# Performance work log

Hardware: AMD Instinct MI355X
Metric: run time of the kernel (lower is better)

## Reference

```python
import jax, jax.numpy as jnp
import numpy as np

TEMPERATURE = 0.1
NUM_CLASSES = 100


def setup_inputs() -> dict:
    key = jax.random.key(0)
    k1, k2 = jax.random.split(key)
    embeddings = jax.random.normal(k1, (8192, 128), dtype=jnp.float32)
    labels = jax.random.randint(k2, (8192,), 0, NUM_CLASSES, dtype=jnp.int64)
    return {"embeddings": embeddings, "labels": labels}


def reference(embeddings, labels):
    # L2-normalize rows (eps matches torch.nn.functional.normalize clamp)
    norm = jnp.maximum(jnp.linalg.norm(embeddings, axis=1, keepdims=True), 1e-12)
    e = embeddings / norm
    sim = jnp.matmul(e, e.T) / TEMPERATURE  # [N, N]
    n = sim.shape[0]
    eye = jnp.eye(n, dtype=bool)
    # positives: same label, excluding self
    pos = (labels[None, :] == labels[:, None]) & ~eye
    # The per-row torch loop computes soft-target cross-entropy over all
    # non-diagonal entries: row_loss_i = -sum_{j in pos(i)} log_softmax(sim[i, j!=i])_j.
    # log_softmax is permutation-invariant, so concatenation order is irrelevant.
    neg_inf = jnp.finfo(sim.dtype).min
    masked = jnp.where(eye, neg_inf, sim)
    logz = jax.nn.logsumexp(masked, axis=1, keepdims=True)  # [N, 1]
    logp = sim - logz  # [N, N]
    row_loss = -jnp.sum(jnp.where(pos, logp, 0.0), axis=1)  # rows with no positives contribute 0
    return jnp.sum(row_loss) / n
```

## Files before the change

### kernel.cpp

```cpp
#include <hip/hip_runtime.h>


#define N 8192
#define D 128
#define NCLS 100
#define JSPLIT 32
#define IBLK 256
#define NJT ((N / JSPLIT) / 16)
#define NPART 8
#define K2E 14.4269504088896340736f
#define LN2 0.69314718055994530942f

typedef __bf16 bf16x8 __attribute__((ext_vector_type(8)));
typedef float f32x4 __attribute__((ext_vector_type(4)));

#define EBF_OFF 0u
#define INV_OFF 0x200000u
#define CNT_OFF 0x208000u
#define Z_OFF   0x208200u
#define SP_OFF  0x210200u
#define ZERO_SZ (512u + 32768u + (NPART * NCLS * D * 4u))

__device__ __forceinline__ unsigned short f32_to_bf16_rne(float f) {
    unsigned int u = __float_as_uint(f);
    u += 0x7fffu + ((u >> 16) & 1u);
    return (unsigned short)(u >> 16);
}


__global__ __launch_bounds__(256) void prep_kernel(
        const float* __restrict__ emb, const int* __restrict__ labels,
        unsigned char* __restrict__ ebf, int* __restrict__ cnt,
        float* __restrict__ spart) {
    const int wave = threadIdx.x >> 6;
    const int lane = threadIdx.x & 63;
    const int row  = blockIdx.x * 4 + wave;

    const float2 v = *(const float2*)(emb + (size_t)row * D + lane * 2);
    float ss = v.x * v.x + v.y * v.y;
    #pragma unroll
    for (int off = 32; off; off >>= 1) ss += __shfl_xor(ss, off);
    const float inv = 1.0f / fmaxf(sqrtf(ss), 1e-12f);
    const float ex = v.x * inv, ey = v.y * inv;

    const int grp = row >> 4, col = row & 15;
    const int c = lane >> 4, q = (lane >> 2) & 3, j2 = lane & 3;
    unsigned int packed = (unsigned int)f32_to_bf16_rne(ex) |
                          ((unsigned int)f32_to_bf16_rne(ey) << 16);
    *(unsigned int*)(ebf + grp * 4096 + c * 1024 + q * 256 + col * 16 + j2 * 4) = packed;

    const int lab = labels[row];
    float* sp = spart + (size_t)(row & (NPART - 1)) * (NCLS * D)
                      + (size_t)lab * D + lane * 2;
    atomicAdd(sp, ex);
    atomicAdd(sp + 1, ey);

    if (lane == 0) atomicAdd(&cnt[lab], 1);
}

__global__ __launch_bounds__(256) void zsum_kernel(
        const unsigned char* __restrict__ ebf, float* __restrict__ z) {
    const int t    = threadIdx.x;
    const int w    = t >> 6;
    const int lane = t & 63;
    const int q    = lane >> 4;
    const int col  = lane & 15;
    const int iw   = blockIdx.x * IBLK + w * 64;
    const int jb   = blockIdx.y * (N / JSPLIT);

    bf16x8 a[4][4];
    #pragma unroll
    for (int g = 0; g < 4; ++g) {
        const unsigned char* ag = ebf + (size_t)(iw / 16 + g) * 4096 + lane * 16;
        #pragma unroll
        for (int c = 0; c < 4; ++c) a[g][c] = *(const bf16x8*)(ag + c * 1024);
    }

    float zacc[4][4] = {{0.f,0.f,0.f,0.f},{0.f,0.f,0.f,0.f},
                        {0.f,0.f,0.f,0.f},{0.f,0.f,0.f,0.f}};

    const unsigned char* bbase = ebf + (size_t)(jb / 16) * 4096 + lane * 16;

    bf16x8 bc[4];
    #pragma unroll
    for (int c = 0; c < 4; ++c) bc[c] = *(const bf16x8*)(bbase + c * 1024);

    #pragma unroll 2
    for (int jt = 0; jt < NJT; ++jt) {
        const int js = jb + jt * 16;

        const int jn = (jt + 1 < NJT) ? jt + 1 : jt;
        bf16x8 bn[4];
        {
            const unsigned char* bg = bbase + (size_t)jn * 4096;
            #pragma unroll
            for (int c = 0; c < 4; ++c) bn[c] = *(const bf16x8*)(bg + c * 1024);
        }

        #pragma unroll
        for (int g = 0; g < 4; ++g) {
            f32x4 acc = {0.f, 0.f, 0.f, 0.f};
            __builtin_amdgcn_s_setprio(1);
            #pragma unroll
            for (int c = 0; c < 4; ++c)
                acc = __builtin_amdgcn_mfma_f32_16x16x32_bf16(a[g][c], bc[c], acc, 0, 0, 0);
            __builtin_amdgcn_s_setprio(0);
            if (js == iw + g * 16) {
                #pragma unroll
                for (int r = 0; r < 4; ++r)
                    zacc[g][r] += (col == q * 4 + r) ? 0.0f
                        : __builtin_amdgcn_exp2f(fmaf(acc[r], K2E, -K2E));
            } else {
                #pragma unroll
                for (int r = 0; r < 4; ++r)
                    zacc[g][r] += __builtin_amdgcn_exp2f(fmaf(acc[r], K2E, -K2E));
            }
        }

        #pragma unroll
        for (int c = 0; c < 4; ++c) bc[c] = bn[c];
    }

    #pragma unroll
    for (int g = 0; g < 4; ++g)
        #pragma unroll
        for (int r = 0; r < 4; ++r) {
            float zv = zacc[g][r];
            zv += __shfl_xor(zv, 1);
            zv += __shfl_xor(zv, 2);
            zv += __shfl_xor(zv, 4);
            zv += __shfl_xor(zv, 8);
            if (col == 0)
                atomicAdd(&z[iw + g * 16 + q * 4 + r], zv);
        }
}

__global__ __launch_bounds__(1024) void final_kernel(
        const int* __restrict__ labels, const int* __restrict__ cnt,
        const float* __restrict__ z, const float* __restrict__ spart,
        float* __restrict__ out) {
    __shared__ float part[16];
    const int tid = threadIdx.x;
    float acc = 0.0f;
    #pragma unroll
    for (int k = 0; k < N / 1024; ++k) {
        const int row = k * 1024 + tid;
        const int P = cnt[labels[row]] - 1;
        if (P > 0)
            acc += (float)P * fmaf(LN2, __builtin_amdgcn_logf(z[row]), 10.0f);
    }
    #pragma unroll
    for (int k = 0; k < (NCLS * D + 1023) / 1024; ++k) {
        const int idx = k * 1024 + tid;
        if (idx < NCLS * D) {
            float sv = 0.0f;
            #pragma unroll
            for (int ch = 0; ch < NPART; ++ch) sv += spart[ch * (NCLS * D) + idx];
            acc -= 10.0f * sv * sv;
        }
    }
    #pragma unroll
    for (int off = 32; off; off >>= 1) acc += __shfl_xor(acc, off);
    if ((tid & 63) == 0) part[tid >> 6] = acc;
    __syncthreads();
    if (tid == 0) {
        float tot = 0.0f;
        #pragma unroll
        for (int w = 0; w < 16; ++w) tot += part[w];
        out[0] = (tot + 10.0f * (float)N) * (1.0f / (float)N);
    }
}

extern "C" void kernel_launch(void* const* d_in, const int* in_sizes, int n_in,
                              void* d_out, int out_size, void* d_ws, size_t ws_size,
                              hipStream_t stream) {
    const float* emb  = (const float*)d_in[0];
    const int* labels = (const int*)d_in[1];
    float* out        = (float*)d_out;
    char* ws          = (char*)d_ws;

    unsigned char* ebf = (unsigned char*)(ws + EBF_OFF);
    int*   cnt         = (int*)(ws + CNT_OFF);
    float* z           = (float*)(ws + Z_OFF);
    float* spart       = (float*)(ws + SP_OFF);

    hipMemsetAsync(ws + CNT_OFF, 0, ZERO_SZ, stream);

    prep_kernel<<<N / 4, 256, 0, stream>>>(emb, labels, ebf, cnt, spart);
    zsum_kernel<<<dim3(N / IBLK, JSPLIT), 256, 0, stream>>>(ebf, z);
    final_kernel<<<1, 1024, 0, stream>>>(labels, cnt, z, spart, out);
}
```

Before: 123.8 us.

## Replace per-class atomic sums with row lists and stage B tiles in LDS

The per-element float atomics that built class sums in the prep kernel are replaced. Prep now writes normalized fp32 rows plus a per-class row list, and a new classsum kernel reduces each class with plain loads. Separately, the zsum kernel stages its whole 64KB B slice into shared memory once per block, so the j-loop reads LDS instead of global memory. The cost is an extra kernel launch, a 4MB enorm buffer, larger LDS use that may limit occupancy, and a class-size cap of 256 that silently drops rows from oversized classes.

```diff
diff --git a/kernel.cpp b/kernel.cpp
--- a/kernel.cpp
+++ b/kernel.cpp
@@ -4,22 +4,23 @@
 #define N 8192
 #define D 128
 #define NCLS 100
+#define RLCAP 256
 #define JSPLIT 32
 #define IBLK 256
 #define NJT ((N / JSPLIT) / 16)
-#define NPART 8
 #define K2E 14.4269504088896340736f
 #define LN2 0.69314718055994530942f
 
 typedef __bf16 bf16x8 __attribute__((ext_vector_type(8)));
 typedef float f32x4 __attribute__((ext_vector_type(4)));
 
-#define EBF_OFF 0u
-#define INV_OFF 0x200000u
-#define CNT_OFF 0x208000u
-#define Z_OFF   0x208200u
-#define SP_OFF  0x210200u
-#define ZERO_SZ (512u + 32768u + (NPART * NCLS * D * 4u))
+#define EBF_OFF  0x000000u
+#define ENORM_OFF 0x200000u
+#define CNT_OFF  0x600000u
+#define Z_OFF    0x600200u
+#define RL_OFF   0x608200u
+#define S_OFF    0x621200u
+#define ZERO_SZ  (512u + 32768u)
 
 __device__ __forceinline__ unsigned short f32_to_bf16_rne(float f) {
     unsigned int u = __float_as_uint(f);
@@ -31,7 +32,7 @@
 __global__ __launch_bounds__(256) void prep_kernel(
         const float* __restrict__ emb, const int* __restrict__ labels,
         unsigned char* __restrict__ ebf, int* __restrict__ cnt,
-        float* __restrict__ spart) {
+        float* __restrict__ enorm, int* __restrict__ rowlist) {
     const int wave = threadIdx.x >> 6;
     const int lane = threadIdx.x & 63;
     const int row  = blockIdx.x * 4 + wave;
@@ -49,17 +50,42 @@
                           ((unsigned int)f32_to_bf16_rne(ey) << 16);
     *(unsigned int*)(ebf + grp * 4096 + c * 1024 + q * 256 + col * 16 + j2 * 4) = packed;
 
-    const int lab = labels[row];
-    float* sp = spart + (size_t)(row & (NPART - 1)) * (NCLS * D)
-                      + (size_t)lab * D + lane * 2;
-    atomicAdd(sp, ex);
-    atomicAdd(sp + 1, ey);
-
-    if (lane == 0) atomicAdd(&cnt[lab], 1);
+    float2* ep = (float2*)(enorm + (size_t)row * D + lane * 2);
+    *ep = make_float2(ex, ey);
+
+    if (lane == 0) {
+        const int lab = labels[row];
+        int slot = atomicAdd(&cnt[lab], 1);
+        slot = slot < RLCAP ? slot : RLCAP - 1;
+        rowlist[lab * RLCAP + slot] = row;
+    }
+}
+
+__global__ __launch_bounds__(128) void classsum_kernel(
+        const float* __restrict__ enorm, const int* __restrict__ cnt,
+        const int* __restrict__ rowlist, float* __restrict__ S) {
+    const int c = blockIdx.x;
+    const int d = threadIdx.x;
+    const int n = cnt[c] < RLCAP ? cnt[c] : RLCAP;
+    const int* rl = rowlist + c * RLCAP;
+    float acc = 0.0f;
+    int idx = 0;
+    for (; idx + 4 <= n; idx += 4) {
+        const int r0 = rl[idx], r1 = rl[idx + 1], r2 = rl[idx + 2], r3 = rl[idx + 3];
+        const float v0 = enorm[(size_t)r0 * D + d];
+        const float v1 = enorm[(size_t)r1 * D + d];
+        const float v2 = enorm[(size_t)r2 * D + d];
+        const float v3 = enorm[(size_t)r3 * D + d];
+        acc += v0 + v1 + v2 + v3;
+    }
+    for (; idx < n; ++idx)
+        acc += enorm[(size_t)rl[idx] * D + d];
+    S[c * D + d] = acc;
 }
 
 __global__ __launch_bounds__(256) void zsum_kernel(
         const unsigned char* __restrict__ ebf, float* __restrict__ z) {
+    __shared__ unsigned char blds[64 * 1024];
     const int t    = threadIdx.x;
     const int w    = t >> 6;
     const int lane = t & 63;
@@ -68,6 +94,18 @@
     const int iw   = blockIdx.x * IBLK + w * 64;
     const int jb   = blockIdx.y * (N / JSPLIT);
 
+    const unsigned char* bsrc = ebf + (size_t)(jb >> 4) * 4096 + lane * 16;
+    #pragma unroll 1
+    for (int kb = 0; kb < 4; ++kb) {
+        bf16x8 tmp[4];
+        #pragma unroll
+        for (int u = 0; u < 4; ++u)
+            tmp[u] = *(const bf16x8*)(bsrc + (size_t)(w * 16 + kb * 4 + u) * 1024);
+        #pragma unroll
+        for (int u = 0; u < 4; ++u)
+            *(bf16x8*)(blds + (w * 16 + kb * 4 + u) * 1024 + lane * 16) = tmp[u];
+    }
+
     bf16x8 a[4][4];
     #pragma unroll
     for (int g = 0; g < 4; ++g) {
@@ -76,26 +114,18 @@
         for (int c = 0; c < 4; ++c) a[g][c] = *(const bf16x8*)(ag + c * 1024);
     }
 
+    __syncthreads();
+
     float zacc[4][4] = {{0.f,0.f,0.f,0.f},{0.f,0.f,0.f,0.f},
                         {0.f,0.f,0.f,0.f},{0.f,0.f,0.f,0.f}};
-
-    const unsigned char* bbase = ebf + (size_t)(jb / 16) * 4096 + lane * 16;
-
-    bf16x8 bc[4];
-    #pragma unroll
-    for (int c = 0; c < 4; ++c) bc[c] = *(const bf16x8*)(bbase + c * 1024);
 
     #pragma unroll 2
     for (int jt = 0; jt < NJT; ++jt) {
         const int js = jb + jt * 16;
-
-        const int jn = (jt + 1 < NJT) ? jt + 1 : jt;
-        bf16x8 bn[4];
-        {
-            const unsigned char* bg = bbase + (size_t)jn * 4096;
-            #pragma unroll
-            for (int c = 0; c < 4; ++c) bn[c] = *(const bf16x8*)(bg + c * 1024);
-        }
+        bf16x8 b[4];
+        #pragma unroll
+        for (int c = 0; c < 4; ++c)
+            b[c] = *(const bf16x8*)(blds + (jt * 4 + c) * 1024 + lane * 16);
 
         #pragma unroll
         for (int g = 0; g < 4; ++g) {
@@ -103,7 +133,7 @@
             __builtin_amdgcn_s_setprio(1);
             #pragma unroll
             for (int c = 0; c < 4; ++c)
-                acc = __builtin_amdgcn_mfma_f32_16x16x32_bf16(a[g][c], bc[c], acc, 0, 0, 0);
+                acc = __builtin_amdgcn_mfma_f32_16x16x32_bf16(a[g][c], b[c], acc, 0, 0, 0);
             __builtin_amdgcn_s_setprio(0);
             if (js == iw + g * 16) {
                 #pragma unroll
@@ -116,9 +146,6 @@
                     zacc[g][r] += __builtin_amdgcn_exp2f(fmaf(acc[r], K2E, -K2E));
             }
         }
-
-        #pragma unroll
-        for (int c = 0; c < 4; ++c) bc[c] = bn[c];
     }
 
     #pragma unroll
@@ -137,7 +164,7 @@
 
 __global__ __launch_bounds__(1024) void final_kernel(
         const int* __restrict__ labels, const int* __restrict__ cnt,
-        const float* __restrict__ z, const float* __restrict__ spart,
+        const float* __restrict__ z, const float* __restrict__ S,
         float* __restrict__ out) {
     __shared__ float part[16];
     const int tid = threadIdx.x;
@@ -153,9 +180,7 @@
     for (int k = 0; k < (NCLS * D + 1023) / 1024; ++k) {
         const int idx = k * 1024 + tid;
         if (idx < NCLS * D) {
-            float sv = 0.0f;
-            #pragma unroll
-            for (int ch = 0; ch < NPART; ++ch) sv += spart[ch * (NCLS * D) + idx];
+            const float sv = S[idx];
             acc -= 10.0f * sv * sv;
         }
     }
@@ -180,13 +205,16 @@
     char* ws          = (char*)d_ws;
 
     unsigned char* ebf = (unsigned char*)(ws + EBF_OFF);
+    float* enorm       = (float*)(ws + ENORM_OFF);
     int*   cnt         = (int*)(ws + CNT_OFF);
     float* z           = (float*)(ws + Z_OFF);
-    float* spart       = (float*)(ws + SP_OFF);
+    int*   rowlist     = (int*)(ws + RL_OFF);
+    float* S           = (float*)(ws + S_OFF);
 
     hipMemsetAsync(ws + CNT_OFF, 0, ZERO_SZ, stream);
 
-    prep_kernel<<<N / 4, 256, 0, stream>>>(emb, labels, ebf, cnt, spart);
+    prep_kernel<<<N / 4, 256, 0, stream>>>(emb, labels, ebf, cnt, enorm, rowlist);
+    classsum_kernel<<<NCLS, 128, 0, stream>>>(enorm, cnt, rowlist, S);
     zsum_kernel<<<dim3(N / IBLK, JSPLIT), 256, 0, stream>>>(ebf, z);
-    final_kernel<<<1, 1024, 0, stream>>>(labels, cnt, z, spart, out);
-}
+    final_kernel<<<1, 1024, 0, stream>>>(labels, cnt, z, S, out);
+}
```

Result: slower. 131.5 us (+6.2%).
